# Performance work log

Measured on AMD Instinct MI355X. Metric: run time of the kernel, lower is better.

The kernel has to match this reference:

```python
import jax, jax.numpy as jnp
import numpy as np

EMBED_DIM = 1024
NUM_HEADS = 16
HEAD_DIM = EMBED_DIM // NUM_HEADS  # 64
BATCH = 4
SEQ_LEN = 2048
TOTAL = BATCH * SEQ_LEN
SOFTMAX_SCALE = 1.0 / np.sqrt(64.0)  # hard-coded 1/sqrt(64) in the source


def setup_inputs() -> dict:
    key = jax.random.key(0)
    ks = jax.random.split(key, 5)
    hidden_states = jax.random.normal(ks[0], (TOTAL, EMBED_DIM), jnp.float32)
    proj_weight = jax.random.normal(ks[1], (3 * EMBED_DIM, EMBED_DIM), jnp.float32) * 0.02
    proj_bias = jax.random.normal(ks[2], (3 * EMBED_DIM,), jnp.float32) * 0.02
    out_weight = jax.random.normal(ks[3], (EMBED_DIM, EMBED_DIM), jnp.float32) * 0.02
    out_bias = jax.random.normal(ks[4], (EMBED_DIM,), jnp.float32) * 0.02
    cu_seqlens = jnp.arange(BATCH + 1, dtype=jnp.int32) * SEQ_LEN
    return {
        "hidden_states": hidden_states,
        "proj_weight": proj_weight,
        "proj_bias": proj_bias,
        "out_weight": out_weight,
        "out_bias": out_bias,
        "cu_seqlens": cu_seqlens,
        "max_len": SEQ_LEN,
    }


def reference(hidden_states, proj_weight, proj_bias, out_weight, out_bias, cu_seqlens, max_len):
    # fused QKV projection: [T, 3E]
    T = hidden_states.shape[0]
    B = cu_seqlens.shape[0] - 1  # static; equal-length packed sequences
    S = T // B
    qkv = hidden_states @ proj_weight.T + proj_bias
    # per-head interleaved layout, matching qkv.view(T, H, 3, D)
    qkv = qkv.reshape(B, S, NUM_HEADS, 3, HEAD_DIM)
    q = qkv[..., 0, :]  # [B, S, H, D]
    k = qkv[..., 1, :]
    v = qkv[..., 2, :]
    scores = jnp.einsum("bqhd,bkhd->bhqk", q, k) * SOFTMAX_SCALE
    attn = jax.nn.softmax(scores, axis=-1)  # non-causal (is_decoder=False)
    ctx = jnp.einsum("bhqk,bkhd->bqhd", attn, v)
    ctx = ctx.reshape(T, NUM_HEADS * HEAD_DIM)
    out = ctx @ out_weight.T + out_bias
    return out
```

## Files before the change

### kernel.cpp

```cpp
#include <hip/hip_runtime.h>
#include <stdint.h>
#include <math.h>


typedef float f32x4 __attribute__((ext_vector_type(4)));
typedef __bf16 bf16x8 __attribute__((ext_vector_type(8)));
typedef __bf16 bf16x4 __attribute__((ext_vector_type(4)));
typedef unsigned short u16x4 __attribute__((ext_vector_type(4)));

#define EMB 1024
#define SEQ 2048
#define NBH 64
#define QSCALE 0.1803368801111204f

__device__ __forceinline__ unsigned short f2bf(float f) {
  unsigned int u = __builtin_bit_cast(unsigned int, f);
  u += 0x7FFFu + ((u >> 16) & 1u);
  return (unsigned short)(u >> 16);
}

__device__ __forceinline__ void gl_lds16(const void* g, void* l) {
  __builtin_amdgcn_global_load_lds(
      (const __attribute__((address_space(1))) unsigned int*)g,
      (__attribute__((address_space(3))) unsigned int*)l, 16, 0, 0);
}

#define N1 2097152u
#define N2 786432u
#define N3 262144u

__global__ __launch_bounds__(256) void convert_k(
    const float* __restrict__ hs, const float* __restrict__ wq,
    const float* __restrict__ wo, unsigned short* __restrict__ hb,
    unsigned short* __restrict__ wqb, unsigned short* __restrict__ wob) {
  unsigned int i = blockIdx.x * 256u + threadIdx.x;
  const float* src; unsigned short* dst; unsigned int off;
  if (i < N1)            { src = hs; dst = hb;  off = i; }
  else if (i < N1 + N2)  { src = wq; dst = wqb; off = i - N1; }
  else                   { src = wo; dst = wob; off = i - (N1 + N2); }
  float4 v = ((const float4*)src)[off];
  u16x4 o;
  o[0] = f2bf(v.x); o[1] = f2bf(v.y); o[2] = f2bf(v.z); o[3] = f2bf(v.w);
  ((u16x4*)dst)[off] = o;
}

template <int EPI>
__global__ __launch_bounds__(256) void gemm_bt(
    const __bf16* __restrict__ A, const __bf16* __restrict__ B,
    const float* __restrict__ bias, float* __restrict__ outF,
    unsigned short* __restrict__ Qg, unsigned short* __restrict__ Kg,
    unsigned short* __restrict__ Vt) {
  __shared__ __bf16 As[128 * 64];
  __shared__ __bf16 Bs[128 * 64];
  const int tid = threadIdx.x;
  const int lane = tid & 63, w = tid >> 6;
  const int wm = w >> 1, wn = w & 1;
  const int l15 = lane & 15, g = lane >> 4;
  const int m0 = blockIdx.y * 128;
  const int n0 = blockIdx.x * 128;

  f32x4 acc[4][4] = {};

  for (int kt = 0; kt < 16; ++kt) {
    const int k0 = kt * 64;
#pragma unroll
    for (int i = 0; i < 4; ++i) {
      int p = i * 256 + tid;
      int row = p >> 3, cp = p & 7;
      int c = cp ^ (row & 7);
      gl_lds16(A + (size_t)(m0 + row) * 1024 + k0 + c * 8, (char*)As + p * 16);
      gl_lds16(B + (size_t)(n0 + row) * 1024 + k0 + c * 8, (char*)Bs + p * 16);
    }
    __syncthreads();
#pragma unroll
    for (int kc = 0; kc < 2; ++kc) {
      bf16x8 af[4], bfr[4];
#pragma unroll
      for (int mf = 0; mf < 4; ++mf) {
        int row = wm * 64 + mf * 16 + l15;
        int c = (kc * 4 + g) ^ (row & 7);
        af[mf] = *(const bf16x8*)((const char*)As + row * 128 + c * 16);
      }
#pragma unroll
      for (int nf = 0; nf < 4; ++nf) {
        int row = wn * 64 + nf * 16 + l15;
        int c = (kc * 4 + g) ^ (row & 7);
        bfr[nf] = *(const bf16x8*)((const char*)Bs + row * 128 + c * 16);
      }
#pragma unroll
      for (int mf = 0; mf < 4; ++mf)
#pragma unroll
        for (int nf = 0; nf < 4; ++nf)
          acc[mf][nf] = __builtin_amdgcn_mfma_f32_16x16x32_bf16(
              af[mf], bfr[nf], acc[mf][nf], 0, 0, 0);
    }
    __syncthreads();
  }

  if (EPI == 0) {
#pragma unroll
    for (int nf = 0; nf < 4; ++nf) {
      int colb = n0 + wn * 64 + nf * 16;
      int h = colb / 192;
      int rb = colb - h * 192;
      int which = rb >> 6;
      int d = (rb & 63) + l15;
      float bv = bias[colb + l15];
#pragma unroll
      for (int mf = 0; mf < 4; ++mf) {
        int t0 = m0 + wm * 64 + mf * 16 + g * 4;
        int b = t0 >> 11, s0 = t0 & 2047;
        size_t bhb = (size_t)(b * 16 + h) * 131072;
        if (which == 2) {
          u16x4 pk;
#pragma unroll
          for (int j = 0; j < 4; ++j) pk[j] = f2bf(acc[mf][nf][j] + bv);
          *(u16x4*)(Vt + bhb + (size_t)d * 2048 + s0) = pk;
        } else {
          unsigned short* dst = (which == 0) ? Qg : Kg;
          float sc = (which == 0) ? QSCALE : 1.0f;
#pragma unroll
          for (int j = 0; j < 4; ++j)
            dst[bhb + (size_t)(s0 + j) * 64 + d] = f2bf((acc[mf][nf][j] + bv) * sc);
        }
      }
    }
  } else {
#pragma unroll
    for (int nf = 0; nf < 4; ++nf) {
      int col = n0 + wn * 64 + nf * 16 + l15;
      float bv = bias[col];
#pragma unroll
      for (int mf = 0; mf < 4; ++mf) {
        int r0 = m0 + wm * 64 + mf * 16 + g * 4;
#pragma unroll
        for (int j = 0; j < 4; ++j)
          outF[(size_t)(r0 + j) * 1024 + col] = acc[mf][nf][j] + bv;
      }
    }
  }
}

__global__ __launch_bounds__(256) void attn_k(
    const __bf16* __restrict__ Qg, const __bf16* __restrict__ Kg,
    const __bf16* __restrict__ Vt, unsigned short* __restrict__ ctxg) {
  __shared__ __bf16 Ks[2][64 * 64];
  __shared__ __bf16 Vs[2][64 * 64];
  __shared__ __bf16 Ps[4][32 * 64];
  const int tid = threadIdx.x;
  const int lane = tid & 63, w = tid >> 6;
  const int l15 = lane & 15, g = lane >> 4;
  const int bh = blockIdx.x >> 4;
  const int qt = blockIdx.x & 15;
  const size_t base = (size_t)bh * 131072;
  const int qbase = qt * 128 + w * 32;

  const int sp0 = tid, sp1 = 256 + tid;
  const int srow0 = sp0 >> 3, sc0 = (sp0 & 7) ^ (srow0 & 7);
  const int srow1 = sp1 >> 3, sc1 = (sp1 & 7) ^ (srow1 & 7);

  bf16x8 qf[2][2];
#pragma unroll
  for (int qs = 0; qs < 2; ++qs)
#pragma unroll
    for (int kc = 0; kc < 2; ++kc)
      qf[qs][kc] = *(const bf16x8*)(Qg + base + (size_t)(qbase + qs * 16 + l15) * 64 +
                                    kc * 32 + g * 8);

  bf16x8 ones;
#pragma unroll
  for (int i = 0; i < 8; ++i) ones[i] = (__bf16)1.0f;

  f32x4 ctx[2][4] = {};
  f32x4 ctx_sum[2] = {};
  char* const pbase_w = (char*)&Ps[w][0];

  gl_lds16(Kg + base + (size_t)srow0 * 64 + sc0 * 8, (char*)&Ks[0][0] + sp0 * 16);
  gl_lds16(Vt + base + (size_t)srow0 * 2048 + sc0 * 8, (char*)&Vs[0][0] + sp0 * 16);
  gl_lds16(Kg + base + (size_t)srow1 * 64 + sc1 * 8, (char*)&Ks[0][0] + sp1 * 16);
  gl_lds16(Vt + base + (size_t)srow1 * 2048 + sc1 * 8, (char*)&Vs[0][0] + sp1 * 16);
  __syncthreads();

  for (int t = 0; t < 32; ++t) {
    const int cur = t & 1;
    const int kb = t * 64;
    const char* const kbuf = (const char*)&Ks[cur][0];
    const char* const vbuf = (const char*)&Vs[cur][0];

    if (t < 31) {
      const int nkb = kb + 64;
      char* const nk = (char*)&Ks[cur ^ 1][0];
      char* const nv = (char*)&Vs[cur ^ 1][0];
      gl_lds16(Kg + base + (size_t)(nkb + srow0) * 64 + sc0 * 8, nk + sp0 * 16);
      gl_lds16(Vt + base + (size_t)srow0 * 2048 + nkb + sc0 * 8, nv + sp0 * 16);
      gl_lds16(Kg + base + (size_t)(nkb + srow1) * 64 + sc1 * 8, nk + sp1 * 16);
      gl_lds16(Vt + base + (size_t)srow1 * 2048 + nkb + sc1 * 8, nv + sp1 * 16);
    }

    f32x4 sc[4][2];
#pragma unroll
    for (int kt4 = 0; kt4 < 4; ++kt4) {
      int krow = kt4 * 16 + l15;
      bf16x8 kf0 = *(const bf16x8*)(kbuf + krow * 128 + ((g ^ (krow & 7)) * 16));
      bf16x8 kf1 = *(const bf16x8*)(kbuf + krow * 128 + (((4 + g) ^ (krow & 7)) * 16));
#pragma unroll
      for (int qs = 0; qs < 2; ++qs) {
        f32x4 a = {0.f, 0.f, 0.f, 0.f};
        a = __builtin_amdgcn_mfma_f32_16x16x32_bf16(kf0, qf[qs][0], a, 0, 0, 0);
        a = __builtin_amdgcn_mfma_f32_16x16x32_bf16(kf1, qf[qs][1], a, 0, 0, 0);
        sc[kt4][qs] = a;
      }
    }

#pragma unroll
    for (int qs = 0; qs < 2; ++qs) {
      int q = qs * 16 + l15;
      char* pb = pbase_w + q * 128;
#pragma unroll
      for (int kt4 = 0; kt4 < 4; ++kt4) {
        int k0 = kt4 * 16 + g * 4;
        bf16x4 pk = {(__bf16)exp2f(sc[kt4][qs][0]),
                     (__bf16)exp2f(sc[kt4][qs][1]),
                     (__bf16)exp2f(sc[kt4][qs][2]),
                     (__bf16)exp2f(sc[kt4][qs][3])};
        *(bf16x4*)(pb + (((k0 >> 3) ^ (q & 7)) * 16) + (k0 & 7) * 2) = pk;
      }
    }

    asm volatile("" ::: "memory");

#pragma unroll
    for (int kc = 0; kc < 2; ++kc) {
      bf16x8 pfr[2], vfr[4];
#pragma unroll
      for (int qs = 0; qs < 2; ++qs) {
        int q = qs * 16 + l15;
        int c = (kc * 4 + g) ^ (q & 7);
        pfr[qs] = *(const bf16x8*)(pbase_w + q * 128 + c * 16);
      }
#pragma unroll
      for (int ds = 0; ds < 4; ++ds) {
        int row = ds * 16 + l15;
        int c = (kc * 4 + g) ^ (row & 7);
        vfr[ds] = *(const bf16x8*)(vbuf + row * 128 + c * 16);
      }
#pragma unroll
      for (int qs = 0; qs < 2; ++qs) {
#pragma unroll
        for (int ds = 0; ds < 4; ++ds)
          ctx[qs][ds] = __builtin_amdgcn_mfma_f32_16x16x32_bf16(
              pfr[qs], vfr[ds], ctx[qs][ds], 0, 0, 0);
        ctx_sum[qs] = __builtin_amdgcn_mfma_f32_16x16x32_bf16(
            pfr[qs], ones, ctx_sum[qs], 0, 0, 0);
      }
    }

    __syncthreads();
  }

  const int b = bh >> 4, h = bh & 15;
#pragma unroll
  for (int qs = 0; qs < 2; ++qs) {
#pragma unroll
    for (int j = 0; j < 4; ++j) {
      float inv = 1.0f / ctx_sum[qs][j];
      int q = qbase + qs * 16 + g * 4 + j;
      size_t trow = (size_t)(b * 2048 + q) * 1024 + h * 64;
#pragma unroll
      for (int ds = 0; ds < 4; ++ds) {
        __bf16 ov = (__bf16)(ctx[qs][ds][j] * inv);
        ctxg[trow + ds * 16 + l15] = __builtin_bit_cast(unsigned short, ov);
      }
    }
  }
}

extern "C" void kernel_launch(void* const* d_in, const int* in_sizes, int n_in,
                              void* d_out, int out_size, void* d_ws, size_t ws_size,
                              hipStream_t stream) {
  (void)in_sizes; (void)n_in; (void)out_size; (void)ws_size;
  const float* hs   = (const float*)d_in[0];
  const float* wqkv = (const float*)d_in[1];
  const float* bqkv = (const float*)d_in[2];
  const float* wout = (const float*)d_in[3];
  const float* bout = (const float*)d_in[4];

  char* ws = (char*)d_ws;
  unsigned short* hb  = (unsigned short*)(ws + 0);
  unsigned short* ctx = (unsigned short*)(ws + 0);
  unsigned short* wqb = (unsigned short*)(ws + 16777216);
  unsigned short* wob = (unsigned short*)(ws + 23068672);
  unsigned short* Qg  = (unsigned short*)(ws + 25165824);
  unsigned short* Kg  = (unsigned short*)(ws + 41943040);
  unsigned short* Vt  = (unsigned short*)(ws + 58720256);

  hipLaunchKernelGGL(convert_k, dim3(12288), dim3(256), 0, stream,
                     hs, wqkv, wout, hb, wqb, wob);
  hipLaunchKernelGGL((gemm_bt<0>), dim3(24, 64), dim3(256), 0, stream,
                     (const __bf16*)hb, (const __bf16*)wqb, bqkv, (float*)nullptr,
                     Qg, Kg, Vt);
  hipLaunchKernelGGL(attn_k, dim3(1024), dim3(256), 0, stream,
                     (const __bf16*)Qg, (const __bf16*)Kg, (const __bf16*)Vt, ctx);
  hipLaunchKernelGGL((gemm_bt<1>), dim3(8, 64), dim3(256), 0, stream,
                     (const __bf16*)ctx, (const __bf16*)wob, bout, (float*)d_out,
                     (unsigned short*)nullptr, (unsigned short*)nullptr,
                     (unsigned short*)nullptr);
}
```

Baseline: 225.1 us.

## Switch attention to 32x32x16 MFMA with register-resident P via permlane swap

Rewrites the attention inner loop to use 32x32x16 bf16 MFMAs instead of 16x16x32. The exponentiated scores stay in registers and are rearranged into A-operand layout with v_permlane32_swap, which removes the per-wave LDS round trip for P. The row sum is now accumulated with scalar adds and combined across half-waves, replacing the extra MFMA against a ones vector. This cuts LDS traffic and MFMA count, at the cost of more register pressure and cross-lane shuffles in the epilogue.

Measured after the change: 228.0 us. About the same (+1.3%).

```diff
diff --git a/kernel.cpp b/kernel.cpp
--- a/kernel.cpp
+++ b/kernel.cpp
@@ -4,8 +4,11 @@
 
 
 typedef float f32x4 __attribute__((ext_vector_type(4)));
+typedef float f32x16 __attribute__((ext_vector_type(16)));
 typedef __bf16 bf16x8 __attribute__((ext_vector_type(8)));
 typedef __bf16 bf16x4 __attribute__((ext_vector_type(4)));
+typedef __bf16 bf16x2 __attribute__((ext_vector_type(2)));
+typedef unsigned int u32x4 __attribute__((ext_vector_type(4)));
 typedef unsigned short u16x4 __attribute__((ext_vector_type(4)));
 
 #define EMB 1024
@@ -17,6 +20,11 @@
   unsigned int u = __builtin_bit_cast(unsigned int, f);
   u += 0x7FFFu + ((u >> 16) & 1u);
   return (unsigned short)(u >> 16);
+}
+
+__device__ __forceinline__ unsigned cvtpk(float a, float b) {
+  bf16x2 v = {(__bf16)a, (__bf16)b};
+  return __builtin_bit_cast(unsigned, v);
 }
 
 __device__ __forceinline__ void gl_lds16(const void* g, void* l) {
@@ -146,39 +154,31 @@
     const __bf16* __restrict__ Vt, unsigned short* __restrict__ ctxg) {
   __shared__ __bf16 Ks[2][64 * 64];
   __shared__ __bf16 Vs[2][64 * 64];
-  __shared__ __bf16 Ps[4][32 * 64];
   const int tid = threadIdx.x;
   const int lane = tid & 63, w = tid >> 6;
-  const int l15 = lane & 15, g = lane >> 4;
+  const int l31 = lane & 31, hi = lane >> 5;
   const int bh = blockIdx.x >> 4;
   const int qt = blockIdx.x & 15;
   const size_t base = (size_t)bh * 131072;
   const int qbase = qt * 128 + w * 32;
 
   const int sp0 = tid, sp1 = 256 + tid;
-  const int srow0 = sp0 >> 3, sc0 = (sp0 & 7) ^ (srow0 & 7);
-  const int srow1 = sp1 >> 3, sc1 = (sp1 & 7) ^ (srow1 & 7);
-
-  bf16x8 qf[2][2];
-#pragma unroll
-  for (int qs = 0; qs < 2; ++qs)
-#pragma unroll
-    for (int kc = 0; kc < 2; ++kc)
-      qf[qs][kc] = *(const bf16x8*)(Qg + base + (size_t)(qbase + qs * 16 + l15) * 64 +
-                                    kc * 32 + g * 8);
-
-  bf16x8 ones;
-#pragma unroll
-  for (int i = 0; i < 8; ++i) ones[i] = (__bf16)1.0f;
-
-  f32x4 ctx[2][4] = {};
-  f32x4 ctx_sum[2] = {};
-  char* const pbase_w = (char*)&Ps[w][0];
-
-  gl_lds16(Kg + base + (size_t)srow0 * 64 + sc0 * 8, (char*)&Ks[0][0] + sp0 * 16);
-  gl_lds16(Vt + base + (size_t)srow0 * 2048 + sc0 * 8, (char*)&Vs[0][0] + sp0 * 16);
-  gl_lds16(Kg + base + (size_t)srow1 * 64 + sc1 * 8, (char*)&Ks[0][0] + sp1 * 16);
-  gl_lds16(Vt + base + (size_t)srow1 * 2048 + sc1 * 8, (char*)&Vs[0][0] + sp1 * 16);
+  const int srow0 = sp0 >> 3, sw0 = (sp0 & 7) ^ (srow0 & 7);
+  const int srow1 = sp1 >> 3, sw1 = (sp1 & 7) ^ (srow1 & 7);
+
+  bf16x8 qf[4];
+#pragma unroll
+  for (int kc = 0; kc < 4; ++kc)
+    qf[kc] = *(const bf16x8*)(Qg + base + (size_t)(qbase + l31) * 64 +
+                              kc * 16 + hi * 8);
+
+  f32x16 ctx0 = {}, ctx1 = {};
+  float ssum = 0.f;
+
+  gl_lds16(Kg + base + (size_t)srow0 * 64 + sw0 * 8, (char*)&Ks[0][0] + sp0 * 16);
+  gl_lds16(Vt + base + (size_t)srow0 * 2048 + sw0 * 8, (char*)&Vs[0][0] + sp0 * 16);
+  gl_lds16(Kg + base + (size_t)srow1 * 64 + sw1 * 8, (char*)&Ks[0][0] + sp1 * 16);
+  gl_lds16(Vt + base + (size_t)srow1 * 2048 + sw1 * 8, (char*)&Vs[0][0] + sp1 * 16);
   __syncthreads();
 
   for (int t = 0; t < 32; ++t) {
@@ -191,87 +191,86 @@
       const int nkb = kb + 64;
       char* const nk = (char*)&Ks[cur ^ 1][0];
       char* const nv = (char*)&Vs[cur ^ 1][0];
-      gl_lds16(Kg + base + (size_t)(nkb + srow0) * 64 + sc0 * 8, nk + sp0 * 16);
-      gl_lds16(Vt + base + (size_t)srow0 * 2048 + nkb + sc0 * 8, nv + sp0 * 16);
-      gl_lds16(Kg + base + (size_t)(nkb + srow1) * 64 + sc1 * 8, nk + sp1 * 16);
-      gl_lds16(Vt + base + (size_t)srow1 * 2048 + nkb + sc1 * 8, nv + sp1 * 16);
-    }
-
-    f32x4 sc[4][2];
-#pragma unroll
-    for (int kt4 = 0; kt4 < 4; ++kt4) {
-      int krow = kt4 * 16 + l15;
-      bf16x8 kf0 = *(const bf16x8*)(kbuf + krow * 128 + ((g ^ (krow & 7)) * 16));
-      bf16x8 kf1 = *(const bf16x8*)(kbuf + krow * 128 + (((4 + g) ^ (krow & 7)) * 16));
-#pragma unroll
-      for (int qs = 0; qs < 2; ++qs) {
-        f32x4 a = {0.f, 0.f, 0.f, 0.f};
-        a = __builtin_amdgcn_mfma_f32_16x16x32_bf16(kf0, qf[qs][0], a, 0, 0, 0);
-        a = __builtin_amdgcn_mfma_f32_16x16x32_bf16(kf1, qf[qs][1], a, 0, 0, 0);
-        sc[kt4][qs] = a;
-      }
-    }
-
-#pragma unroll
-    for (int qs = 0; qs < 2; ++qs) {
-      int q = qs * 16 + l15;
-      char* pb = pbase_w + q * 128;
-#pragma unroll
-      for (int kt4 = 0; kt4 < 4; ++kt4) {
-        int k0 = kt4 * 16 + g * 4;
-        bf16x4 pk = {(__bf16)exp2f(sc[kt4][qs][0]),
-                     (__bf16)exp2f(sc[kt4][qs][1]),
-                     (__bf16)exp2f(sc[kt4][qs][2]),
-                     (__bf16)exp2f(sc[kt4][qs][3])};
-        *(bf16x4*)(pb + (((k0 >> 3) ^ (q & 7)) * 16) + (k0 & 7) * 2) = pk;
-      }
-    }
-
-    asm volatile("" ::: "memory");
-
-#pragma unroll
-    for (int kc = 0; kc < 2; ++kc) {
-      bf16x8 pfr[2], vfr[4];
-#pragma unroll
-      for (int qs = 0; qs < 2; ++qs) {
-        int q = qs * 16 + l15;
-        int c = (kc * 4 + g) ^ (q & 7);
-        pfr[qs] = *(const bf16x8*)(pbase_w + q * 128 + c * 16);
-      }
-#pragma unroll
-      for (int ds = 0; ds < 4; ++ds) {
-        int row = ds * 16 + l15;
-        int c = (kc * 4 + g) ^ (row & 7);
-        vfr[ds] = *(const bf16x8*)(vbuf + row * 128 + c * 16);
-      }
-#pragma unroll
-      for (int qs = 0; qs < 2; ++qs) {
-#pragma unroll
-        for (int ds = 0; ds < 4; ++ds)
-          ctx[qs][ds] = __builtin_amdgcn_mfma_f32_16x16x32_bf16(
-              pfr[qs], vfr[ds], ctx[qs][ds], 0, 0, 0);
-        ctx_sum[qs] = __builtin_amdgcn_mfma_f32_16x16x32_bf16(
-            pfr[qs], ones, ctx_sum[qs], 0, 0, 0);
+      gl_lds16(Kg + base + (size_t)(nkb + srow0) * 64 + sw0 * 8, nk + sp0 * 16);
+      gl_lds16(Vt + base + (size_t)srow0 * 2048 + nkb + sw0 * 8, nv + sp0 * 16);
+      gl_lds16(Kg + base + (size_t)(nkb + srow1) * 64 + sw1 * 8, nk + sp1 * 16);
+      gl_lds16(Vt + base + (size_t)srow1 * 2048 + nkb + sw1 * 8, nv + sp1 * 16);
+    }
+
+    f32x16 sc32[2];
+#pragma unroll
+    for (int kblk = 0; kblk < 2; ++kblk) {
+      const int row = kblk * 32 + l31;
+      const char* const krow = kbuf + row * 128;
+      const int sw = row & 7;
+      f32x16 a = {};
+#pragma unroll
+      for (int kc = 0; kc < 4; ++kc) {
+        bf16x8 kf = *(const bf16x8*)(krow + (((kc * 2 + hi) ^ sw) * 16));
+        a = __builtin_amdgcn_mfma_f32_32x32x16_bf16(kf, qf[kc], a, 0, 0, 0);
+      }
+      sc32[kblk] = a;
+    }
+
+    u32x4 pa[4];
+    float ts = 0.f;
+#pragma unroll
+    for (int kblk = 0; kblk < 2; ++kblk) {
+      float p[16];
+#pragma unroll
+      for (int r = 0; r < 16; ++r) p[r] = exp2f(sc32[kblk][r]);
+#pragma unroll
+      for (int r = 0; r < 16; r += 4)
+        ts += (p[r] + p[r + 1]) + (p[r + 2] + p[r + 3]);
+      unsigned pk[8];
+#pragma unroll
+      for (int r2 = 0; r2 < 8; ++r2) pk[r2] = cvtpk(p[2 * r2], p[2 * r2 + 1]);
+#pragma unroll
+      for (int c = 0; c < 2; ++c) {
+        unsigned a0 = pk[c * 4 + 0], b0 = pk[c * 4 + 2];
+        unsigned a1 = pk[c * 4 + 1], b1 = pk[c * 4 + 3];
+        asm("v_permlane32_swap_b32 %0, %1" : "+v"(a0), "+v"(b0));
+        asm("v_permlane32_swap_b32 %0, %1" : "+v"(a1), "+v"(b1));
+        u32x4 af = {a0, a1, b0, b1};
+        pa[kblk * 2 + c] = af;
+      }
+    }
+    ssum += ts;
+
+#pragma unroll
+    for (int kc = 0; kc < 4; ++kc) {
+      bf16x8 paf = __builtin_bit_cast(bf16x8, pa[kc]);
+      {
+        const int d = l31;
+        bf16x8 vf = *(const bf16x8*)(vbuf + d * 128 + (((kc * 2 + hi) ^ (d & 7)) * 16));
+        ctx0 = __builtin_amdgcn_mfma_f32_32x32x16_bf16(paf, vf, ctx0, 0, 0, 0);
+      }
+      {
+        const int d = 32 + l31;
+        bf16x8 vf = *(const bf16x8*)(vbuf + d * 128 + (((kc * 2 + hi) ^ (d & 7)) * 16));
+        ctx1 = __builtin_amdgcn_mfma_f32_32x32x16_bf16(paf, vf, ctx1, 0, 0, 0);
       }
     }
 
     __syncthreads();
   }
 
+  float sa = ssum, sb = ssum;
+  asm("v_permlane32_swap_b32 %0, %1" : "+v"(sa), "+v"(sb));
+  float total = ssum + (hi ? sa : sb);
+  float inv = 1.0f / total;
+
   const int b = bh >> 4, h = bh & 15;
 #pragma unroll
-  for (int qs = 0; qs < 2; ++qs) {
-#pragma unroll
-    for (int j = 0; j < 4; ++j) {
-      float inv = 1.0f / ctx_sum[qs][j];
-      int q = qbase + qs * 16 + g * 4 + j;
-      size_t trow = (size_t)(b * 2048 + q) * 1024 + h * 64;
-#pragma unroll
-      for (int ds = 0; ds < 4; ++ds) {
-        __bf16 ov = (__bf16)(ctx[qs][ds][j] * inv);
-        ctxg[trow + ds * 16 + l15] = __builtin_bit_cast(unsigned short, ov);
-      }
-    }
+  for (int r = 0; r < 16; ++r) {
+    const int qrow = (r & 3) + 8 * (r >> 2) + 4 * hi;
+    float invr = __shfl(inv, qrow);
+    const int q = qbase + qrow;
+    size_t trow = (size_t)(b * 2048 + q) * 1024 + h * 64 + l31;
+    __bf16 o0 = (__bf16)(ctx0[r] * invr);
+    __bf16 o1 = (__bf16)(ctx1[r] * invr);
+    ctxg[trow] = __builtin_bit_cast(unsigned short, o0);
+    ctxg[trow + 32] = __builtin_bit_cast(unsigned short, o1);
   }
 }
 
```
